# Performance work log

Hardware: AMD Instinct MI355X
Metric: run time of the kernel (lower is better)

Reference implementation:

```python
import jax, jax.numpy as jnp
import numpy as np

NEG_SLOPE = 0.2  # self.alpha


def setup_inputs() -> dict:
    key = jax.random.key(0)
    k1, k2, k3, k4 = jax.random.split(key, 4)
    N, E, in_dim, out_dim = 50000, 800000, 128, 64
    inp = jax.random.normal(k1, (N, in_dim), dtype=jnp.float32)
    edge = jax.random.randint(k2, (2, E), 0, N, dtype=jnp.int64)
    # xavier_normal init scales
    W = jax.random.normal(k3, (in_dim, out_dim), dtype=jnp.float32) * np.sqrt(2.0 / (in_dim + out_dim))
    a = jax.random.normal(k4, (2 * out_dim, 1), dtype=jnp.float32) * np.sqrt(2.0 / (2 * out_dim + 1))
    return {"input": inp, "edge": edge, "W": W, "a": a}


def reference(input, edge, W, a):
    # eval mode: dropout is a no-op
    N = input.shape[0]
    h = input @ W                           # [N, out_dim]
    src, dst = edge[0], edge[1]             # [E], [E]
    out_dim = h.shape[1]
    a_src, a_dst = a[:out_dim, 0], a[out_dim:, 0]
    # equivalent to cat([h[src], h[dst]], 1) @ a, without materializing [E, 2*out_dim]
    score = (h @ a_src)[src] + (h @ a_dst)[dst]          # [E]
    e = jax.nn.leaky_relu(score, negative_slope=NEG_SLOPE)
    # sparse softmax over each row (segment by src)
    m = jax.ops.segment_max(e, src, num_segments=N)      # [N], -inf for empty rows
    m = jnp.where(jnp.isfinite(m), m, 0.0)
    ex = jnp.exp(e - m[src])                             # [E]
    s = jax.ops.segment_sum(ex, src, num_segments=N)     # [N]
    attn = ex / s[src]                                   # [E]
    # scatter-aggregate: out[i] = sum_{(i,j) in E} attn_ij * h[j]
    out = jax.ops.segment_sum(attn[:, None] * h[dst], src, num_segments=N)  # [N, out_dim]
    return jax.nn.elu(out)
```

## Files before the change

kernel.cpp:

```cpp
#include <hip/hip_runtime.h>
#include <hip/hip_fp16.h>
#include <math.h>

#define IN_DIM 128
#define OUT_DIM 64
#define NEG_SLOPE 0.2f

#define BUCKET_SRCS 32
#define CAP 1024
#define MAXBK 2048

typedef _Float16 half8 __attribute__((ext_vector_type(8)));
typedef float floatx4 __attribute__((ext_vector_type(4)));

#define GR 64

__global__ __launch_bounds__(256) void gemm_hs_hd(
    const float* __restrict__ in, const float* __restrict__ W,
    const float* __restrict__ a, __half* __restrict__ hb,
    float* __restrict__ hs, float* __restrict__ hd,
    int* __restrict__ zero_base, int zero_n, int N)
{
    __shared__ _Float16 Al[GR][IN_DIM];
    __shared__ _Float16 Wt[OUT_DIM][IN_DIM + 8];
    __shared__ _Float16 Crep[GR][OUT_DIM + 8];

    const int t = threadIdx.x;
    for (int i = blockIdx.x * 256 + t; i < zero_n; i += gridDim.x * 256)
        zero_base[i] = 0;

    const int r0 = blockIdx.x * GR;

    #pragma unroll
    for (int i = 0; i < 8; ++i) {
        int q = i * 256 + t;
        int row = q >> 5;
        int kq  = (q & 31) * 4;
        int grow = r0 + row; if (grow >= N) grow = N - 1;
        float4 v = *(const float4*)&in[(size_t)grow * IN_DIM + kq];
        union { __half2 h2[2]; uint2 u; } cv;
        cv.h2[0] = __floats2half2_rn(v.x, v.y);
        cv.h2[1] = __floats2half2_rn(v.z, v.w);
        *(uint2*)&Al[row][kq] = cv.u;
    }
    #pragma unroll
    for (int i = 0; i < 8; ++i) {
        int q = i * 256 + t;
        int k  = q >> 4;
        int n4 = (q & 15) * 4;
        float4 v = *(const float4*)&W[(size_t)k * OUT_DIM + n4];
        Wt[n4 + 0][k] = (_Float16)v.x;
        Wt[n4 + 1][k] = (_Float16)v.y;
        Wt[n4 + 2][k] = (_Float16)v.z;
        Wt[n4 + 3][k] = (_Float16)v.w;
    }
    __syncthreads();

    const int lane = t & 63;
    const int wave = t >> 6;
    const int m16  = lane & 15;
    const int quad = lane >> 4;

    floatx4 acc[4];
    #pragma unroll
    for (int nt = 0; nt < 4; ++nt) acc[nt] = (floatx4){0.f, 0.f, 0.f, 0.f};

    #pragma unroll
    for (int kc = 0; kc < 4; ++kc) {
        half8 af = *(const half8*)&Al[wave * 16 + m16][kc * 32 + quad * 8];
        #pragma unroll
        for (int nt = 0; nt < 4; ++nt) {
            half8 bf = *(const half8*)&Wt[nt * 16 + m16][kc * 32 + quad * 8];
            acc[nt] = __builtin_amdgcn_mfma_f32_16x16x32_f16(af, bf, acc[nt], 0, 0, 0);
        }
    }

    float asl[4], adl[4];
    #pragma unroll
    for (int nt = 0; nt < 4; ++nt) {
        asl[nt] = a[nt * 16 + m16];
        adl[nt] = a[OUT_DIM + nt * 16 + m16];
    }
    #pragma unroll
    for (int r = 0; r < 4; ++r) {
        float ps = 0.f, pd = 0.f;
        #pragma unroll
        for (int nt = 0; nt < 4; ++nt) {
            ps = fmaf(acc[nt][r], asl[nt], ps);
            pd = fmaf(acc[nt][r], adl[nt], pd);
        }
        #pragma unroll
        for (int off = 1; off < 16; off <<= 1) {
            ps += __shfl_xor(ps, off, 64);
            pd += __shfl_xor(pd, off, 64);
        }
        if (m16 == 0) {
            int row = r0 + wave * 16 + quad * 4 + r;
            if (row < N) { hs[row] = ps; hd[row] = pd; }
        }
    }

    #pragma unroll
    for (int nt = 0; nt < 4; ++nt)
        #pragma unroll
        for (int r = 0; r < 4; ++r)
            Crep[wave * 16 + quad * 4 + r][nt * 16 + m16] = (_Float16)acc[nt][r];
    __syncthreads();
    #pragma unroll
    for (int i = 0; i < 2; ++i) {
        int idx = i * 256 + t;
        int row = idx >> 3;
        int seg = idx & 7;
        int gr2 = r0 + row;
        if (gr2 < N) {
            uint4 v = *(const uint4*)&Crep[row][seg * 8];
            *(uint4*)&hb[(size_t)gr2 * OUT_DIM + seg * 8] = v;
        }
    }
}

#define PA_CHUNK 4096
__global__ __launch_bounds__(256) void partition_kernel(
    const int* __restrict__ src, const int* __restrict__ dst,
    int* __restrict__ gcursor, int* __restrict__ pairbuf, int E, int NBK)
{
    __shared__ int lcount[MAXBK];
    __shared__ int lbase[MAXBK];
    __shared__ int lrun[MAXBK];
    const int t = threadIdx.x;
    for (int i = t; i < NBK; i += 256) lcount[i] = 0;
    __syncthreads();

    const int base = blockIdx.x * PA_CHUNK;
    int pk[16], b[16];
    int nloc = 0;
    #pragma unroll
    for (int j = 0; j < 16; ++j) {
        int i = base + j * 256 + t;
        if (i < E) {
            int s = src[i];
            b[j]  = s >> 5;
            pk[j] = ((s & 31) << 16) | dst[i];
            atomicAdd(&lcount[b[j]], 1);
            nloc = j + 1;
        }
    }
    __syncthreads();
    for (int i = t; i < NBK; i += 256) {
        int c = lcount[i];
        int gb = 0;
        if (c > 0) gb = atomicAdd(&gcursor[i], c);
        lbase[i] = i * CAP + gb;
        lrun[i] = 0;
    }
    __syncthreads();
    for (int j = 0; j < nloc; ++j) {
        int r = atomicAdd(&lrun[b[j]], 1);
        int pos = lbase[b[j]] + r;
        if (pos - b[j] * CAP < CAP)
            pairbuf[pos] = pk[j];
    }
}

__global__ __launch_bounds__(256) void node_kernel(
    const __half* __restrict__ hb, const float* __restrict__ hs,
    const float* __restrict__ hd, const int* __restrict__ gcursor,
    const int* __restrict__ pairbuf, float* __restrict__ out, int N)
{
    __shared__ int2  spair[CAP];
    __shared__ float hsl[BUCKET_SRCS];
    __shared__ int   cnt[BUCKET_SRCS];
    __shared__ int   excl[BUCKET_SRCS];
    __shared__ int   lcur[BUCKET_SRCS];

    const int t = threadIdx.x;
    const int b = blockIdx.x;
    const int M = min(gcursor[b], CAP);

    if (t < BUCKET_SRCS) {
        int node = b * BUCKET_SRCS + t;
        hsl[t] = (node < N) ? hs[node] : 0.f;
        cnt[t] = 0;
    }
    __syncthreads();

    int   dloc[CAP / 256], slv[CAP / 256];
    float exv[CAP / 256];
    int nl = 0;
    #pragma unroll
    for (int j = 0; j < CAP / 256; ++j) {
        int i = j * 256 + t;
        if (i < M) {
            int pk = pairbuf[b * CAP + i];
            int sl = (pk >> 16) & 31;
            int d  = pk & 0xffff;
            float e = hsl[sl] + hd[d];
            e = (e >= 0.f) ? e : NEG_SLOPE * e;
            float ex = __expf(e);
            atomicAdd(&cnt[sl], 1);
            dloc[j] = d; slv[j] = sl; exv[j] = ex;
            nl = j + 1;
        }
    }
    __syncthreads();
    if (t < BUCKET_SRCS) {
        int raw = cnt[t];
        int v = raw;
        #pragma unroll
        for (int off = 1; off < BUCKET_SRCS; off <<= 1) {
            int u = __shfl_up(v, off, 64);
            if (t >= off) v += u;
        }
        excl[t] = v - raw;
        lcur[t] = v - raw;
    }
    __syncthreads();
    for (int j = 0; j < nl; ++j) {
        int r = atomicAdd(&lcur[slv[j]], 1);
        spair[r] = make_int2(__float_as_int(exv[j]), dloc[j]);
    }
    __syncthreads();

    const int lane = t & 63;
    const int wave = t >> 6;
    const int slot = lane >> 3;
    const int c8   = lane & 7;
    const int loc  = wave * 8 + slot;
    const int node = b * BUCKET_SRCS + loc;
    const bool valid = node < N;

    const int deg = cnt[loc];
    const int beg = excl[loc];

    int dmax = deg;
    #pragma unroll
    for (int off = 8; off < 64; off <<= 1)
        dmax = max(dmax, __shfl_xor(dmax, off, 64));

    float acc[8];
    float ssum = 0.f;
    #pragma unroll
    for (int q = 0; q < 8; ++q) acc[q] = 0.f;

    for (int j = 0; j < dmax; j += 2) {
        bool a0 = j < deg;
        bool a1 = j + 1 < deg;
        int2 pr0 = spair[beg + (a0 ? j : 0)];
        int2 pr1 = spair[beg + (a1 ? j + 1 : 0)];
        float ex0 = a0 ? __int_as_float(pr0.x) : 0.f;
        float ex1 = a1 ? __int_as_float(pr1.x) : 0.f;
        ssum += ex0 + ex1;
        union { uint4 u; __half2 h2[4]; } hv0, hv1;
        hv0.u = *(const uint4*)&hb[(size_t)pr0.y * OUT_DIM + c8 * 8];
        hv1.u = *(const uint4*)&hb[(size_t)pr1.y * OUT_DIM + c8 * 8];
        #pragma unroll
        for (int q = 0; q < 4; ++q) {
            acc[2 * q]     = fmaf(ex0, __low2float(hv0.h2[q]),  acc[2 * q]);
            acc[2 * q + 1] = fmaf(ex0, __high2float(hv0.h2[q]), acc[2 * q + 1]);
        }
        #pragma unroll
        for (int q = 0; q < 4; ++q) {
            acc[2 * q]     = fmaf(ex1, __low2float(hv1.h2[q]),  acc[2 * q]);
            acc[2 * q + 1] = fmaf(ex1, __high2float(hv1.h2[q]), acc[2 * q + 1]);
        }
    }

    if (valid) {
        float inv = (deg > 0) ? 1.f / ssum : 0.f;
        float o[8];
        #pragma unroll
        for (int q = 0; q < 8; ++q) {
            float v = acc[q] * inv;
            o[q] = (v > 0.f) ? v : (__expf(v) - 1.f);
        }
        float4 o0 = {o[0], o[1], o[2], o[3]};
        float4 o1 = {o[4], o[5], o[6], o[7]};
        *(float4*)&out[(size_t)node * OUT_DIM + c8 * 8] = o0;
        *(float4*)&out[(size_t)node * OUT_DIM + c8 * 8 + 4] = o1;
    }
}

extern "C" void kernel_launch(void* const* d_in, const int* in_sizes, int n_in,
                              void* d_out, int out_size, void* d_ws, size_t ws_size,
                              hipStream_t stream)
{
    const float* input = (const float*)d_in[0];
    const int*   edge  = (const int*)d_in[1];
    const float* W     = (const float*)d_in[2];
    const float* a     = (const float*)d_in[3];
    float* out = (float*)d_out;

    const int N = in_sizes[0] / IN_DIM;
    const int E = in_sizes[1] / 2;
    const int* src = edge;
    const int* dst = edge + E;

    const int NBK = (N + BUCKET_SRCS - 1) / BUCKET_SRCS;

    size_t idx = 0;
    int* gcursor = (int*)d_ws + idx; idx += MAXBK;
    int* pairbuf = (int*)d_ws + idx; idx += (size_t)NBK * CAP;
    __half* hb = (__half*)((int*)d_ws + idx); idx += (size_t)N * OUT_DIM / 2;
    float* hs = (float*)((int*)d_ws + idx); idx += N;
    float* hd = (float*)((int*)d_ws + idx); idx += N;

    gemm_hs_hd<<<(N + GR - 1) / GR, 256, 0, stream>>>(
        input, W, a, hb, hs, hd, gcursor, NBK, N);
    partition_kernel<<<(E + PA_CHUNK - 1) / PA_CHUNK, 256, 0, stream>>>(
        src, dst, gcursor, pairbuf, E, NBK);
    node_kernel<<<NBK, 256, 0, stream>>>(hb, hs, hd, gcursor, pairbuf, out, N);
}
```

Before: 119.2 us.

## Fuse GEMM and edge partition into one kernel with block-range dispatch

Merges the feature GEMM kernel and the edge bucketing/partition kernel into a single launch, with the first PB blocks doing partitioning and the rest doing the GEMM, sharing LDS through a union. This removes one kernel launch and the serialization between two independent stages so they can run concurrently on the GPU. Zeroing of the bucket cursors moves to a hipMemsetAsync, and the Crep staging buffer now reuses the Al region behind an added barrier. The extra memset is still a separate stream operation, and the union sizes LDS to the larger of the two stages for every block.

```diff
diff --git a/kernel.cpp b/kernel.cpp
--- a/kernel.cpp
+++ b/kernel.cpp
@@ -14,22 +14,60 @@
 typedef float floatx4 __attribute__((ext_vector_type(4)));
 
 #define GR 64
-
-__global__ __launch_bounds__(256) void gemm_hs_hd(
+#define PA_CHUNK 4096
+
+__global__ __launch_bounds__(256) void fused_gp(
     const float* __restrict__ in, const float* __restrict__ W,
     const float* __restrict__ a, __half* __restrict__ hb,
     float* __restrict__ hs, float* __restrict__ hd,
-    int* __restrict__ zero_base, int zero_n, int N)
+    const int* __restrict__ src, const int* __restrict__ dst,
+    int* __restrict__ gcursor, int* __restrict__ pairbuf,
+    int E, int NBK, int PB, int N)
 {
-    __shared__ _Float16 Al[GR][IN_DIM];
-    __shared__ _Float16 Wt[OUT_DIM][IN_DIM + 8];
-    __shared__ _Float16 Crep[GR][OUT_DIM + 8];
+    __shared__ union {
+        struct { _Float16 Al[GR][IN_DIM]; _Float16 Wt[OUT_DIM][IN_DIM + 8]; } g;
+        struct { int lcount[MAXBK]; int lbase[MAXBK]; int lrun[MAXBK]; } p;
+    } sm;
 
     const int t = threadIdx.x;
-    for (int i = blockIdx.x * 256 + t; i < zero_n; i += gridDim.x * 256)
-        zero_base[i] = 0;
-
-    const int r0 = blockIdx.x * GR;
+
+    if ((int)blockIdx.x < PB) {
+        for (int i = t; i < NBK; i += 256) sm.p.lcount[i] = 0;
+        __syncthreads();
+
+        const int base = blockIdx.x * PA_CHUNK;
+        int pk[16], b[16];
+        int nloc = 0;
+        #pragma unroll
+        for (int j = 0; j < 16; ++j) {
+            int i = base + j * 256 + t;
+            if (i < E) {
+                int s = src[i];
+                b[j]  = s >> 5;
+                pk[j] = ((s & 31) << 16) | dst[i];
+                atomicAdd(&sm.p.lcount[b[j]], 1);
+                nloc = j + 1;
+            }
+        }
+        __syncthreads();
+        for (int i = t; i < NBK; i += 256) {
+            int c = sm.p.lcount[i];
+            int gb = 0;
+            if (c > 0) gb = atomicAdd(&gcursor[i], c);
+            sm.p.lbase[i] = i * CAP + gb;
+            sm.p.lrun[i] = 0;
+        }
+        __syncthreads();
+        for (int j = 0; j < nloc; ++j) {
+            int r = atomicAdd(&sm.p.lrun[b[j]], 1);
+            int pos = sm.p.lbase[b[j]] + r;
+            if (pos - b[j] * CAP < CAP)
+                pairbuf[pos] = pk[j];
+        }
+        return;
+    }
+
+    const int r0 = (blockIdx.x - PB) * GR;
 
     #pragma unroll
     for (int i = 0; i < 8; ++i) {
@@ -41,7 +79,7 @@
         union { __half2 h2[2]; uint2 u; } cv;
         cv.h2[0] = __floats2half2_rn(v.x, v.y);
         cv.h2[1] = __floats2half2_rn(v.z, v.w);
-        *(uint2*)&Al[row][kq] = cv.u;
+        *(uint2*)&sm.g.Al[row][kq] = cv.u;
     }
     #pragma unroll
     for (int i = 0; i < 8; ++i) {
@@ -49,10 +87,10 @@
         int k  = q >> 4;
         int n4 = (q & 15) * 4;
         float4 v = *(const float4*)&W[(size_t)k * OUT_DIM + n4];
-        Wt[n4 + 0][k] = (_Float16)v.x;
-        Wt[n4 + 1][k] = (_Float16)v.y;
-        Wt[n4 + 2][k] = (_Float16)v.z;
-        Wt[n4 + 3][k] = (_Float16)v.w;
+        sm.g.Wt[n4 + 0][k] = (_Float16)v.x;
+        sm.g.Wt[n4 + 1][k] = (_Float16)v.y;
+        sm.g.Wt[n4 + 2][k] = (_Float16)v.z;
+        sm.g.Wt[n4 + 3][k] = (_Float16)v.w;
     }
     __syncthreads();
 
@@ -67,13 +105,16 @@
 
     #pragma unroll
     for (int kc = 0; kc < 4; ++kc) {
-        half8 af = *(const half8*)&Al[wave * 16 + m16][kc * 32 + quad * 8];
+        half8 af = *(const half8*)&sm.g.Al[wave * 16 + m16][kc * 32 + quad * 8];
         #pragma unroll
         for (int nt = 0; nt < 4; ++nt) {
-            half8 bf = *(const half8*)&Wt[nt * 16 + m16][kc * 32 + quad * 8];
+            half8 bf = *(const half8*)&sm.g.Wt[nt * 16 + m16][kc * 32 + quad * 8];
             acc[nt] = __builtin_amdgcn_mfma_f32_16x16x32_f16(af, bf, acc[nt], 0, 0, 0);
         }
     }
+    __syncthreads();
+
+    _Float16 (*Crep)[OUT_DIM + 8] = (_Float16(*)[OUT_DIM + 8])&sm.g.Al[0][0];
 
     float asl[4], adl[4];
     #pragma unroll
@@ -116,49 +157,6 @@
             uint4 v = *(const uint4*)&Crep[row][seg * 8];
             *(uint4*)&hb[(size_t)gr2 * OUT_DIM + seg * 8] = v;
         }
-    }
-}
-
-#define PA_CHUNK 4096
-__global__ __launch_bounds__(256) void partition_kernel(
-    const int* __restrict__ src, const int* __restrict__ dst,
-    int* __restrict__ gcursor, int* __restrict__ pairbuf, int E, int NBK)
-{
-    __shared__ int lcount[MAXBK];
-    __shared__ int lbase[MAXBK];
-    __shared__ int lrun[MAXBK];
-    const int t = threadIdx.x;
-    for (int i = t; i < NBK; i += 256) lcount[i] = 0;
-    __syncthreads();
-
-    const int base = blockIdx.x * PA_CHUNK;
-    int pk[16], b[16];
-    int nloc = 0;
-    #pragma unroll
-    for (int j = 0; j < 16; ++j) {
-        int i = base + j * 256 + t;
-        if (i < E) {
-            int s = src[i];
-            b[j]  = s >> 5;
-            pk[j] = ((s & 31) << 16) | dst[i];
-            atomicAdd(&lcount[b[j]], 1);
-            nloc = j + 1;
-        }
-    }
-    __syncthreads();
-    for (int i = t; i < NBK; i += 256) {
-        int c = lcount[i];
-        int gb = 0;
-        if (c > 0) gb = atomicAdd(&gcursor[i], c);
-        lbase[i] = i * CAP + gb;
-        lrun[i] = 0;
-    }
-    __syncthreads();
-    for (int j = 0; j < nloc; ++j) {
-        int r = atomicAdd(&lrun[b[j]], 1);
-        int pos = lbase[b[j]] + r;
-        if (pos - b[j] * CAP < CAP)
-            pairbuf[pos] = pk[j];
     }
 }
 
@@ -296,6 +294,8 @@
     const int* dst = edge + E;
 
     const int NBK = (N + BUCKET_SRCS - 1) / BUCKET_SRCS;
+    const int PB  = (E + PA_CHUNK - 1) / PA_CHUNK;
+    const int GB  = (N + GR - 1) / GR;
 
     size_t idx = 0;
     int* gcursor = (int*)d_ws + idx; idx += MAXBK;
@@ -304,9 +304,8 @@
     float* hs = (float*)((int*)d_ws + idx); idx += N;
     float* hd = (float*)((int*)d_ws + idx); idx += N;
 
-    gemm_hs_hd<<<(N + GR - 1) / GR, 256, 0, stream>>>(
-        input, W, a, hb, hs, hd, gcursor, NBK, N);
-    partition_kernel<<<(E + PA_CHUNK - 1) / PA_CHUNK, 256, 0, stream>>>(
-        src, dst, gcursor, pairbuf, E, NBK);
+    hipMemsetAsync(gcursor, 0, MAXBK * sizeof(int), stream);
+    fused_gp<<<PB + GB, 256, 0, stream>>>(
+        input, W, a, hb, hs, hd, src, dst, gcursor, pairbuf, E, NBK, PB, N);
     node_kernel<<<NBK, 256, 0, stream>>>(hb, hs, hd, gcursor, pairbuf, out, N);
 }
```

After: 113.4 us. 4.9% less time.
